# Kernel tuning notes

Measured on AMD Instinct MI355X. Metric: run time of the kernel, lower is better.

The kernel has to match this reference:

```python
import jax, jax.numpy as jnp
import numpy as np
from jax import lax

EPOCHS = 10  # self.epoch in the torch module


def setup_inputs() -> dict:
    key = jax.random.key(0)
    k1, k2 = jax.random.split(key)
    # (num_patches, groups, channels_per_group, kh, kw)
    patches = jax.random.normal(k1, (40000, 4, 16, 5, 5), dtype=jnp.float32)
    # torch: torch.randn([groups, K, D]) * 0.1
    centroids_init = jax.random.normal(k2, (4, 64, 400), dtype=jnp.float32) * 0.1
    return {"patches": patches, "centroids_init": centroids_init}


def reference(patches, centroids_init):
    N, G, C, H, W = patches.shape
    K = centroids_init.shape[1]
    D = C * H * W
    # [G, N, D] flattened patches per group
    pf = jnp.transpose(patches.reshape(N, G, D), (1, 0, 2))

    def step(centroids, _):
        # half squared norm of each centroid: [G, K]
        c2 = 0.5 * jnp.sum(centroids * centroids, axis=2)
        # scores[g,n,k] = <c_gk, p_gn> - 0.5||c_gk||^2  (max over k == nearest centroid)
        scores = jnp.einsum('gkd,gnd->gnk', centroids, pf) - c2[:, None, :]
        labels = jnp.argmax(scores, axis=2)                       # [G, N]
        S = jax.nn.one_hot(labels, K, dtype=pf.dtype)             # [G, N, K]
        summation = jnp.einsum('gnk,gnd->gkd', S, pf)             # [G, K, D]
        counts = jnp.sum(S, axis=1)                               # [G, K]
        new_c = summation / jnp.where(counts == 0, 1.0, counts)[:, :, None]
        # torch: centroids[:, where(counts==0)[1], :] = 0  -> zero that cluster
        # index across ALL groups if empty in any group
        bad = jnp.any(counts == 0, axis=0)                        # [K]
        new_c = jnp.where(bad[None, :, None], 0.0, new_c)
        return new_c, None

    centroids, _ = lax.scan(step, centroids_init, None, length=EPOCHS)
    # reshape to conv weight layout (out_channels, channels_per_group, kh, kw)
    return centroids.reshape(G * K, C, H, W)
```

## Files before the change

### kernel.cpp

```cpp
#include <hip/hip_runtime.h>

#define NPTS   40000
#define NG     4
#define NK     64
#define ND     400
#define PT     128
#define NCHUNK 25
#define NTILES 313
#define NSPL   16

typedef _Float16 f16x4 __attribute__((ext_vector_type(4)));
typedef float    f32x4 __attribute__((ext_vector_type(4)));

__global__ __launch_bounds__(256)
void assign_kernel(const float* __restrict__ patches,
                   const float* __restrict__ cent,
                   int*   __restrict__ lr,
                   int*   __restrict__ pcnt)
{
    const int g    = blockIdx.y;
    const int tile = blockIdx.x;
    const int t    = threadIdx.x;
    const int n0   = tile * PT;

    __shared__ _Float16 A1[PT][20];
    __shared__ _Float16 A2[PT][20];
    __shared__ _Float16 B1[NK][20];
    __shared__ _Float16 B2[NK][20];
    __shared__ float c2p[NK][4];
    __shared__ float c2s[NK];
    __shared__ int   cnt[NK];

    if (t < NK) cnt[t] = 0;

    {
        int k = t >> 2, j = t & 3;
        const float* c = cent + ((size_t)g * NK + k) * ND + 100 * j;
        float s = 0.0f;
        #pragma unroll
        for (int d = 0; d < 100; d += 4) {
            float4 v = *(const float4*)(c + d);
            s = fmaf(v.x, v.x, fmaf(v.y, v.y, fmaf(v.z, v.z, fmaf(v.w, v.w, s))));
        }
        c2p[k][j] = s;
    }
    __syncthreads();
    if (t < NK) c2s[t] = 2048.0f * (c2p[t][0] + c2p[t][1] + c2p[t][2] + c2p[t][3]);

    const int w   = t >> 6;
    const int l   = t & 63;
    const int q   = l >> 4;
    const int r15 = l & 15;

    const int rh = t & 127;
    const int hh = t >> 7;
    int nn = n0 + rh; if (nn >= NPTS) nn = NPTS - 1;
    const float* prow = patches + ((size_t)nn * NG + g) * ND + 8 * hh;
    const float* crow = cent + ((size_t)g * NK + (t >> 2)) * ND + 4 * (t & 3);

    f32x4 acc[2][4];
    {
        f32x4 z = {0.f, 0.f, 0.f, 0.f};
        #pragma unroll
        for (int i = 0; i < 2; ++i)
            #pragma unroll
            for (int j = 0; j < 4; ++j) acc[i][j] = z;
    }

    float4 pp[2]; float4 pc;
    pp[0] = *(const float4*)(prow);
    pp[1] = *(const float4*)(prow + 4);
    pc = *(const float4*)(crow);

    for (int c = 0; c < NCHUNK; ++c) {
        #pragma unroll
        for (int j2 = 0; j2 < 2; ++j2) {
            float4 v = pp[j2];
            float s0 = v.x * 64.0f, s1 = v.y * 64.0f, s2 = v.z * 64.0f, s3 = v.w * 64.0f;
            _Float16 a0 = (_Float16)s0, a1 = (_Float16)s1, a2 = (_Float16)s2, a3 = (_Float16)s3;
            f16x4 h1 = {a0, a1, a2, a3};
            f16x4 h2 = {(_Float16)(s0 - (float)a0), (_Float16)(s1 - (float)a1),
                        (_Float16)(s2 - (float)a2), (_Float16)(s3 - (float)a3)};
            *(f16x4*)&A1[rh][8 * hh + 4 * j2] = h1;
            *(f16x4*)&A2[rh][8 * hh + 4 * j2] = h2;
        }
        {
            float4 v = pc;
            float s0 = v.x * 64.0f, s1 = v.y * 64.0f, s2 = v.z * 64.0f, s3 = v.w * 64.0f;
            _Float16 a0 = (_Float16)s0, a1 = (_Float16)s1, a2 = (_Float16)s2, a3 = (_Float16)s3;
            f16x4 h1 = {a0, a1, a2, a3};
            f16x4 h2 = {(_Float16)(s0 - (float)a0), (_Float16)(s1 - (float)a1),
                        (_Float16)(s2 - (float)a2), (_Float16)(s3 - (float)a3)};
            int cc = t >> 2, jj = t & 3;
            *(f16x4*)&B1[cc][4 * jj] = h1;
            *(f16x4*)&B2[cc][4 * jj] = h2;
        }
        __syncthreads();

        if (c + 1 < NCHUNK) {
            const int d0 = (c + 1) * 16;
            pp[0] = *(const float4*)(prow + d0);
            pp[1] = *(const float4*)(prow + d0 + 4);
            pc = *(const float4*)(crow + d0);
        }

        f16x4 a1v[2], a2v[2], b1v[4], b2v[4];
        #pragma unroll
        for (int pi = 0; pi < 2; ++pi) {
            int p = 32 * w + 16 * pi + r15;
            a1v[pi] = *(const f16x4*)&A1[p][4 * q];
            a2v[pi] = *(const f16x4*)&A2[p][4 * q];
        }
        #pragma unroll
        for (int cj = 0; cj < 4; ++cj) {
            int n = 16 * cj + r15;
            b1v[cj] = *(const f16x4*)&B1[n][4 * q];
            b2v[cj] = *(const f16x4*)&B2[n][4 * q];
        }
        #pragma unroll
        for (int pi = 0; pi < 2; ++pi)
            #pragma unroll
            for (int cj = 0; cj < 4; ++cj) {
                acc[pi][cj] = __builtin_amdgcn_mfma_f32_16x16x16f16(a2v[pi], b1v[cj], acc[pi][cj], 0, 0, 0);
                acc[pi][cj] = __builtin_amdgcn_mfma_f32_16x16x16f16(a1v[pi], b2v[cj], acc[pi][cj], 0, 0, 0);
                acc[pi][cj] = __builtin_amdgcn_mfma_f32_16x16x16f16(a1v[pi], b1v[cj], acc[pi][cj], 0, 0, 0);
            }
        __syncthreads();
    }

    #pragma unroll
    for (int pi = 0; pi < 2; ++pi) {
        #pragma unroll
        for (int r = 0; r < 4; ++r) {
            float m  = acc[pi][0][r] - c2s[r15];
            int best = r15;
            #pragma unroll
            for (int cj = 1; cj < 4; ++cj) {
                int n = 16 * cj + r15;
                float s = acc[pi][cj][r] - c2s[n];
                if (s > m) { m = s; best = n; }
            }
            #pragma unroll
            for (int off = 1; off < 16; off <<= 1) {
                float om = __shfl_xor(m, off);
                int   ob = __shfl_xor(best, off);
                if (om > m || (om == m && ob < best)) { m = om; best = ob; }
            }
            if (r15 == 0) {
                int p  = 32 * w + 16 * pi + 4 * q + r;
                int np = n0 + p;
                if (np < NPTS) {
                    int rk = atomicAdd(&cnt[best], 1);
                    lr[(size_t)g * NPTS + np] = (rk << 8) | best;
                }
            }
        }
    }
    __syncthreads();
    if (t < NK) pcnt[((size_t)g * NTILES + tile) * NK + t] = cnt[t];
}

__global__ __launch_bounds__(256)
void scatter2_kernel(const int* __restrict__ lr,
                     const int* __restrict__ pcnt,
                     int* __restrict__ order,
                     int* __restrict__ cbase,
                     int* __restrict__ counts)
{
    const int tile = blockIdx.x, g = blockIdx.y, t = threadIdx.x;
    __shared__ unsigned short cnt_tk[NTILES * NK];
    __shared__ int part [4][NK];
    __shared__ int part2[4][NK];
    __shared__ int kbase[NK];
    __shared__ int tpre[NK];

    const int* pg = pcnt + (size_t)g * NTILES * NK;
    for (int i = t; i < NTILES * NK; i += 256)
        cnt_tk[i] = (unsigned short)pg[i];
    __syncthreads();

    {
        int k = t & 63, p = t >> 6;
        int s1 = 0, s2 = 0;
        for (int tl = p; tl < NTILES; tl += 4) {
            int v = cnt_tk[tl * NK + k];
            s1 += v;
            if (tl < tile) s2 += v;
        }
        part [p][k] = s1;
        part2[p][k] = s2;
    }
    __syncthreads();
    if (t < NK) {
        part[0][t] = part[0][t] + part[1][t] + part[2][t] + part[3][t];
        tpre[t]    = part2[0][t] + part2[1][t] + part2[2][t] + part2[3][t];
    }
    __syncthreads();
    if (t == 0) {
        int run = 0;
        for (int k = 0; k < NK; ++k) { kbase[k] = run; run += part[0][k]; }
    }
    __syncthreads();
    if (tile == 0 && t < NK) {
        cbase[g * NK + t]  = kbase[t];
        counts[g * NK + t] = part[0][t];
    }
    const int n = tile * PT + t;
    if (t < PT && n < NPTS) {
        int packed = lr[(size_t)g * NPTS + n];
        int L = packed & 63, r = packed >> 8;
        order[(size_t)g * NPTS + kbase[L] + tpre[L] + r] = n;
    }
}

__global__ __launch_bounds__(512, 2)
void gather_kernel(const float* __restrict__ patches,
                   const int*   __restrict__ order,
                   const int*   __restrict__ cbase,
                   const int*   __restrict__ counts,
                   float* __restrict__ psum)
{
    const int s = blockIdx.x, k = blockIdx.y, g = blockIdx.z;
    const int t = threadIdx.x;
    const int base = cbase[g * NK + k];
    const int cnt  = counts[g * NK + k];
    const int start = base + (cnt * s) / NSPL;
    const int end   = base + (cnt * (s + 1)) / NSPL;

    const int slot = t / 100;
    const int q    = t - slot * 100;

    float4 acc = make_float4(0.f, 0.f, 0.f, 0.f);
    if (t < 500) {
        const int* ord = order + (size_t)g * NPTS;
        #pragma unroll 4
        for (int i = start + slot; i < end; i += 5) {
            int n = ord[i];
            float4 v = *(const float4*)(patches + ((size_t)n * NG + g) * ND + 4 * q);
            acc.x += v.x; acc.y += v.y; acc.z += v.z; acc.w += v.w;
        }
    }

    __shared__ float sums[ND];
    for (int i = t; i < ND; i += 512) sums[i] = 0.0f;
    __syncthreads();
    if (t < 500) {
        atomicAdd(&sums[4 * q + 0], acc.x);
        atomicAdd(&sums[4 * q + 1], acc.y);
        atomicAdd(&sums[4 * q + 2], acc.z);
        atomicAdd(&sums[4 * q + 3], acc.w);
    }
    __syncthreads();
    if (t < 100) {
        float* dst = psum + (((size_t)(g * NK + k)) * NSPL + s) * ND + 4 * t;
        *(float4*)dst = *(const float4*)&sums[4 * t];
    }
}

__global__ __launch_bounds__(128)
void update_kernel(const float* __restrict__ psum,
                   const int*   __restrict__ counts,
                   float* __restrict__ outc)
{
    const int gk = blockIdx.x;
    const int g = gk >> 6, k = gk & 63;
    const int t = threadIdx.x;

    const bool bad = (counts[0 * NK + k] == 0) | (counts[1 * NK + k] == 0) |
                     (counts[2 * NK + k] == 0) | (counts[3 * NK + k] == 0);
    const int  c  = counts[g * NK + k];
    const float inv = 1.0f / (float)(c == 0 ? 1 : c);

    if (t < 100) {
        float4 s = make_float4(0.f, 0.f, 0.f, 0.f);
        const float* p = psum + ((size_t)gk * NSPL) * ND + 4 * t;
        #pragma unroll
        for (int sp = 0; sp < NSPL; ++sp) {
            float4 v = *(const float4*)(p + (size_t)sp * ND);
            s.x += v.x; s.y += v.y; s.z += v.z; s.w += v.w;
        }
        float4 o;
        o.x = bad ? 0.0f : s.x * inv;
        o.y = bad ? 0.0f : s.y * inv;
        o.z = bad ? 0.0f : s.z * inv;
        o.w = bad ? 0.0f : s.w * inv;
        *(float4*)(outc + (size_t)gk * ND + 4 * t) = o;
    }
}

extern "C" void kernel_launch(void* const* d_in, const int* in_sizes, int n_in,
                              void* d_out, int out_size, void* d_ws, size_t ws_size,
                              hipStream_t stream)
{
    const float* patches = (const float*)d_in[0];
    const float* cinit   = (const float*)d_in[1];
    float* out = (float*)d_out;

    const size_t CSZ = (size_t)NG * NK * ND;
    float* centA = (float*)d_ws;
    float* centB = centA + CSZ;
    int* lr       = (int*)(centB + CSZ);
    int* pcnt     = lr + (size_t)NG * NPTS;
    int* cbase    = pcnt + (size_t)NG * NTILES * NK;
    int* counts   = cbase + NG * NK;
    int* order    = counts + NG * NK;
    float* psum   = (float*)(order + (size_t)NG * NPTS);

    const float* cur = cinit;
    for (int e = 0; e < 10; ++e) {
        assign_kernel<<<dim3(NTILES, NG), 256, 0, stream>>>(patches, cur, lr, pcnt);
        scatter2_kernel<<<dim3(NTILES, NG), 256, 0, stream>>>(lr, pcnt, order, cbase, counts);
        gather_kernel<<<dim3(NSPL, NK, NG), 512, 0, stream>>>(patches, order, cbase, counts, psum);
        float* nxt = (e == 9) ? out : ((e & 1) ? centB : centA);
        update_kernel<<<dim3(NG * NK), 128, 0, stream>>>(psum, counts, nxt);
        cur = nxt;
    }
}
```

Measured before the change: 1.723 ms.

## Precompute fp16 hi/lo patch split and replace per-tile count scan with global atomics

Adds a one-time prepass that converts patches into scaled fp16 hi/lo pairs. The assign and gather kernels read these pairs directly, so the split is no longer recomputed in every epoch. Update writes the next centroids in the same split form. Cluster ranks now come from global atomic counters, which removes the per-tile count buffer and the heavy scan in which every scatter block reread all tile counts. The cost is an extra full pass over patches up front, contention on 256 global counters, and a point order within each cluster that is no longer deterministic.

Result: slower. 4.297 ms (+149.4%).

```diff
diff --git a/kernel.cpp b/kernel.cpp
--- a/kernel.cpp
+++ b/kernel.cpp
@@ -4,6 +4,7 @@
 #define NG     4
 #define NK     64
 #define ND     400
+#define NQ     100
 #define PT     128
 #define NCHUNK 25
 #define NTILES 313
@@ -12,11 +13,41 @@
 typedef _Float16 f16x4 __attribute__((ext_vector_type(4)));
 typedef float    f32x4 __attribute__((ext_vector_type(4)));
 
+struct __align__(16) HL { f16x4 hi; f16x4 lo; };
+
+__device__ __forceinline__ HL split4(float4 v) {
+    float s0 = v.x * 64.0f, s1 = v.y * 64.0f, s2 = v.z * 64.0f, s3 = v.w * 64.0f;
+    _Float16 a0 = (_Float16)s0, a1 = (_Float16)s1, a2 = (_Float16)s2, a3 = (_Float16)s3;
+    HL h;
+    h.hi = f16x4{a0, a1, a2, a3};
+    h.lo = f16x4{(_Float16)(s0 - (float)a0), (_Float16)(s1 - (float)a1),
+                 (_Float16)(s2 - (float)a2), (_Float16)(s3 - (float)a3)};
+    return h;
+}
+
 __global__ __launch_bounds__(256)
-void assign_kernel(const float* __restrict__ patches,
+void prepass_kernel(const float* __restrict__ patches, HL* __restrict__ ps)
+{
+    const int total = NPTS * NG * NQ;
+    for (int i = blockIdx.x * 256 + threadIdx.x; i < total; i += gridDim.x * 256)
+        ps[i] = split4(((const float4*)patches)[i]);
+}
+
+__global__ __launch_bounds__(128)
+void centprep_kernel(const float* __restrict__ cent, HL* __restrict__ cs,
+                     int* __restrict__ gcntbuf)
+{
+    const int gk = blockIdx.x, t = threadIdx.x;
+    if (t < NQ) cs[gk * NQ + t] = split4(((const float4*)cent)[gk * NQ + t]);
+    if (gk < 20 && t < 128) gcntbuf[gk * 128 + t] = 0;
+}
+
+__global__ __launch_bounds__(256)
+void assign_kernel(const HL* __restrict__ ps,
                    const float* __restrict__ cent,
+                   const HL* __restrict__ cs,
                    int*   __restrict__ lr,
-                   int*   __restrict__ pcnt)
+                   int*   __restrict__ gcnt)
 {
     const int g    = blockIdx.y;
     const int tile = blockIdx.x;
@@ -29,9 +60,6 @@
     __shared__ _Float16 B2[NK][20];
     __shared__ float c2p[NK][4];
     __shared__ float c2s[NK];
-    __shared__ int   cnt[NK];
-
-    if (t < NK) cnt[t] = 0;
 
     {
         int k = t >> 2, j = t & 3;
@@ -55,8 +83,9 @@
     const int rh = t & 127;
     const int hh = t >> 7;
     int nn = n0 + rh; if (nn >= NPTS) nn = NPTS - 1;
-    const float* prow = patches + ((size_t)nn * NG + g) * ND + 8 * hh;
-    const float* crow = cent + ((size_t)g * NK + (t >> 2)) * ND + 4 * (t & 3);
+    const HL* prow = ps + ((size_t)nn * NG + g) * NQ;
+    const HL* crow = cs + ((size_t)g * NK + (t >> 2)) * NQ;
+    const int jj = t & 3;
 
     f32x4 acc[2][4];
     {
@@ -67,41 +96,27 @@
             for (int j = 0; j < 4; ++j) acc[i][j] = z;
     }
 
-    float4 pp[2]; float4 pc;
-    pp[0] = *(const float4*)(prow);
-    pp[1] = *(const float4*)(prow + 4);
-    pc = *(const float4*)(crow);
+    HL ha0 = prow[2 * hh];
+    HL ha1 = prow[2 * hh + 1];
+    HL hb  = crow[jj];
 
     for (int c = 0; c < NCHUNK; ++c) {
-        #pragma unroll
-        for (int j2 = 0; j2 < 2; ++j2) {
-            float4 v = pp[j2];
-            float s0 = v.x * 64.0f, s1 = v.y * 64.0f, s2 = v.z * 64.0f, s3 = v.w * 64.0f;
-            _Float16 a0 = (_Float16)s0, a1 = (_Float16)s1, a2 = (_Float16)s2, a3 = (_Float16)s3;
-            f16x4 h1 = {a0, a1, a2, a3};
-            f16x4 h2 = {(_Float16)(s0 - (float)a0), (_Float16)(s1 - (float)a1),
-                        (_Float16)(s2 - (float)a2), (_Float16)(s3 - (float)a3)};
-            *(f16x4*)&A1[rh][8 * hh + 4 * j2] = h1;
-            *(f16x4*)&A2[rh][8 * hh + 4 * j2] = h2;
-        }
+        *(f16x4*)&A1[rh][8 * hh]     = ha0.hi;
+        *(f16x4*)&A2[rh][8 * hh]     = ha0.lo;
+        *(f16x4*)&A1[rh][8 * hh + 4] = ha1.hi;
+        *(f16x4*)&A2[rh][8 * hh + 4] = ha1.lo;
         {
-            float4 v = pc;
-            float s0 = v.x * 64.0f, s1 = v.y * 64.0f, s2 = v.z * 64.0f, s3 = v.w * 64.0f;
-            _Float16 a0 = (_Float16)s0, a1 = (_Float16)s1, a2 = (_Float16)s2, a3 = (_Float16)s3;
-            f16x4 h1 = {a0, a1, a2, a3};
-            f16x4 h2 = {(_Float16)(s0 - (float)a0), (_Float16)(s1 - (float)a1),
-                        (_Float16)(s2 - (float)a2), (_Float16)(s3 - (float)a3)};
-            int cc = t >> 2, jj = t & 3;
-            *(f16x4*)&B1[cc][4 * jj] = h1;
-            *(f16x4*)&B2[cc][4 * jj] = h2;
+            int cc = t >> 2;
+            *(f16x4*)&B1[cc][4 * jj] = hb.hi;
+            *(f16x4*)&B2[cc][4 * jj] = hb.lo;
         }
         __syncthreads();
 
         if (c + 1 < NCHUNK) {
-            const int d0 = (c + 1) * 16;
-            pp[0] = *(const float4*)(prow + d0);
-            pp[1] = *(const float4*)(prow + d0 + 4);
-            pc = *(const float4*)(crow + d0);
+            const int q0 = 4 * (c + 1);
+            ha0 = prow[q0 + 2 * hh];
+            ha1 = prow[q0 + 2 * hh + 1];
+            hb  = crow[q0 + jj];
         }
 
         f16x4 a1v[2], a2v[2], b1v[4], b2v[4];
@@ -150,80 +165,51 @@
                 int p  = 32 * w + 16 * pi + 4 * q + r;
                 int np = n0 + p;
                 if (np < NPTS) {
-                    int rk = atomicAdd(&cnt[best], 1);
-                    lr[(size_t)g * NPTS + np] = (rk << 8) | best;
+                    int rk = atomicAdd(&gcnt[g * NK + best], 1);
+                    lr[(size_t)g * NPTS + np] = (rk << 6) | best;
                 }
             }
         }
     }
-    __syncthreads();
-    if (t < NK) pcnt[((size_t)g * NTILES + tile) * NK + t] = cnt[t];
-}
-
-__global__ __launch_bounds__(256)
-void scatter2_kernel(const int* __restrict__ lr,
-                     const int* __restrict__ pcnt,
-                     int* __restrict__ order,
-                     int* __restrict__ cbase,
-                     int* __restrict__ counts)
+}
+
+__global__ __launch_bounds__(128)
+void scatter_kernel(const int* __restrict__ lr,
+                    const int* __restrict__ gcnt,
+                    int* __restrict__ order)
 {
     const int tile = blockIdx.x, g = blockIdx.y, t = threadIdx.x;
-    __shared__ unsigned short cnt_tk[NTILES * NK];
-    __shared__ int part [4][NK];
-    __shared__ int part2[4][NK];
-    __shared__ int kbase[NK];
-    __shared__ int tpre[NK];
-
-    const int* pg = pcnt + (size_t)g * NTILES * NK;
-    for (int i = t; i < NTILES * NK; i += 256)
-        cnt_tk[i] = (unsigned short)pg[i];
-    __syncthreads();
-
-    {
-        int k = t & 63, p = t >> 6;
-        int s1 = 0, s2 = 0;
-        for (int tl = p; tl < NTILES; tl += 4) {
-            int v = cnt_tk[tl * NK + k];
-            s1 += v;
-            if (tl < tile) s2 += v;
-        }
-        part [p][k] = s1;
-        part2[p][k] = s2;
-    }
-    __syncthreads();
-    if (t < NK) {
-        part[0][t] = part[0][t] + part[1][t] + part[2][t] + part[3][t];
-        tpre[t]    = part2[0][t] + part2[1][t] + part2[2][t] + part2[3][t];
-    }
-    __syncthreads();
+    __shared__ int kb[NK];
     if (t == 0) {
         int run = 0;
-        for (int k = 0; k < NK; ++k) { kbase[k] = run; run += part[0][k]; }
-    }
-    __syncthreads();
-    if (tile == 0 && t < NK) {
-        cbase[g * NK + t]  = kbase[t];
-        counts[g * NK + t] = part[0][t];
-    }
+        for (int k = 0; k < NK; ++k) { kb[k] = run; run += gcnt[g * NK + k]; }
+    }
+    __syncthreads();
     const int n = tile * PT + t;
-    if (t < PT && n < NPTS) {
+    if (n < NPTS) {
         int packed = lr[(size_t)g * NPTS + n];
-        int L = packed & 63, r = packed >> 8;
-        order[(size_t)g * NPTS + kbase[L] + tpre[L] + r] = n;
+        int L = packed & 63, r = packed >> 6;
+        order[(size_t)g * NPTS + kb[L] + r] = n;
     }
 }
 
 __global__ __launch_bounds__(512, 2)
-void gather_kernel(const float* __restrict__ patches,
-                   const int*   __restrict__ order,
-                   const int*   __restrict__ cbase,
-                   const int*   __restrict__ counts,
+void gather_kernel(const HL*  __restrict__ ps,
+                   const int* __restrict__ order,
+                   const int* __restrict__ gcnt,
                    float* __restrict__ psum)
 {
     const int s = blockIdx.x, k = blockIdx.y, g = blockIdx.z;
     const int t = threadIdx.x;
-    const int base = cbase[g * NK + k];
-    const int cnt  = counts[g * NK + k];
+
+    __shared__ int sb[2];
+    if (t == 0) {
+        int b = 0;
+        for (int i = 0; i < k; ++i) b += gcnt[g * NK + i];
+        sb[0] = b; sb[1] = gcnt[g * NK + k];
+    }
+    __syncthreads();
+    const int base = sb[0], cnt = sb[1];
     const int start = base + (cnt * s) / NSPL;
     const int end   = base + (cnt * (s + 1)) / NSPL;
 
@@ -233,11 +219,14 @@
     float4 acc = make_float4(0.f, 0.f, 0.f, 0.f);
     if (t < 500) {
         const int* ord = order + (size_t)g * NPTS;
-        #pragma unroll 4
+        #pragma unroll 2
         for (int i = start + slot; i < end; i += 5) {
             int n = ord[i];
-            float4 v = *(const float4*)(patches + ((size_t)n * NG + g) * ND + 4 * q);
-            acc.x += v.x; acc.y += v.y; acc.z += v.z; acc.w += v.w;
+            HL h = ps[((size_t)n * NG + g) * NQ + q];
+            acc.x += (float)h.hi[0] + (float)h.lo[0];
+            acc.y += (float)h.hi[1] + (float)h.lo[1];
+            acc.z += (float)h.hi[2] + (float)h.lo[2];
+            acc.w += (float)h.hi[3] + (float)h.lo[3];
         }
     }
 
@@ -259,19 +248,20 @@
 
 __global__ __launch_bounds__(128)
 void update_kernel(const float* __restrict__ psum,
-                   const int*   __restrict__ counts,
-                   float* __restrict__ outc)
+                   const int*   __restrict__ gcnt,
+                   float* __restrict__ outc,
+                   HL*    __restrict__ cs)
 {
     const int gk = blockIdx.x;
     const int g = gk >> 6, k = gk & 63;
     const int t = threadIdx.x;
 
-    const bool bad = (counts[0 * NK + k] == 0) | (counts[1 * NK + k] == 0) |
-                     (counts[2 * NK + k] == 0) | (counts[3 * NK + k] == 0);
-    const int  c  = counts[g * NK + k];
+    const bool bad = (gcnt[0 * NK + k] == 0) | (gcnt[1 * NK + k] == 0) |
+                     (gcnt[2 * NK + k] == 0) | (gcnt[3 * NK + k] == 0);
+    const int  c  = gcnt[g * NK + k];
     const float inv = 1.0f / (float)(c == 0 ? 1 : c);
 
-    if (t < 100) {
+    if (t < NQ) {
         float4 s = make_float4(0.f, 0.f, 0.f, 0.f);
         const float* p = psum + ((size_t)gk * NSPL) * ND + 4 * t;
         #pragma unroll
@@ -279,12 +269,21 @@
             float4 v = *(const float4*)(p + (size_t)sp * ND);
             s.x += v.x; s.y += v.y; s.z += v.z; s.w += v.w;
         }
-        float4 o;
-        o.x = bad ? 0.0f : s.x * inv;
-        o.y = bad ? 0.0f : s.y * inv;
-        o.z = bad ? 0.0f : s.z * inv;
-        o.w = bad ? 0.0f : s.w * inv;
+        float4 c64;
+        c64.x = bad ? 0.0f : s.x * inv;
+        c64.y = bad ? 0.0f : s.y * inv;
+        c64.z = bad ? 0.0f : s.z * inv;
+        c64.w = bad ? 0.0f : s.w * inv;
+        float4 o = make_float4(c64.x * 0.015625f, c64.y * 0.015625f,
+                               c64.z * 0.015625f, c64.w * 0.015625f);
         *(float4*)(outc + (size_t)gk * ND + 4 * t) = o;
+        _Float16 a0 = (_Float16)c64.x, a1 = (_Float16)c64.y,
+                 a2 = (_Float16)c64.z, a3 = (_Float16)c64.w;
+        HL h;
+        h.hi = f16x4{a0, a1, a2, a3};
+        h.lo = f16x4{(_Float16)(c64.x - (float)a0), (_Float16)(c64.y - (float)a1),
+                     (_Float16)(c64.z - (float)a2), (_Float16)(c64.w - (float)a3)};
+        cs[(size_t)gk * NQ + t] = h;
     }
 }
 
@@ -296,23 +295,27 @@
     const float* cinit   = (const float*)d_in[1];
     float* out = (float*)d_out;
 
-    const size_t CSZ = (size_t)NG * NK * ND;
-    float* centA = (float*)d_ws;
-    float* centB = centA + CSZ;
-    int* lr       = (int*)(centB + CSZ);
-    int* pcnt     = lr + (size_t)NG * NPTS;
-    int* cbase    = pcnt + (size_t)NG * NTILES * NK;
-    int* counts   = cbase + NG * NK;
-    int* order    = counts + NG * NK;
-    float* psum   = (float*)(order + (size_t)NG * NPTS);
+    char* wp = (char*)d_ws;
+    HL* PS = (HL*)wp;               wp += (size_t)NPTS * NG * NQ * sizeof(HL);
+    HL* CS = (HL*)wp;               wp += (size_t)NG * NK * NQ * sizeof(HL);
+    float* centA = (float*)wp;      wp += (size_t)NG * NK * ND * 4;
+    float* centB = (float*)wp;      wp += (size_t)NG * NK * ND * 4;
+    int* lr      = (int*)wp;        wp += (size_t)NG * NPTS * 4;
+    int* order   = (int*)wp;        wp += (size_t)NG * NPTS * 4;
+    int* gcntbuf = (int*)wp;        wp += 2560 * 4;
+    float* psum  = (float*)wp;
+
+    prepass_kernel<<<4096, 256, 0, stream>>>(patches, PS);
+    centprep_kernel<<<NG * NK, 128, 0, stream>>>(cinit, CS, gcntbuf);
 
     const float* cur = cinit;
     for (int e = 0; e < 10; ++e) {
-        assign_kernel<<<dim3(NTILES, NG), 256, 0, stream>>>(patches, cur, lr, pcnt);
-        scatter2_kernel<<<dim3(NTILES, NG), 256, 0, stream>>>(lr, pcnt, order, cbase, counts);
-        gather_kernel<<<dim3(NSPL, NK, NG), 512, 0, stream>>>(patches, order, cbase, counts, psum);
+        int* gc = gcntbuf + 256 * e;
+        assign_kernel<<<dim3(NTILES, NG), 256, 0, stream>>>(PS, cur, CS, lr, gc);
+        scatter_kernel<<<dim3(NTILES, NG), 128, 0, stream>>>(lr, gc, order);
+        gather_kernel<<<dim3(NSPL, NK, NG), 512, 0, stream>>>(PS, order, gc, psum);
         float* nxt = (e == 9) ? out : ((e & 1) ? centB : centA);
-        update_kernel<<<dim3(NG * NK), 128, 0, stream>>>(psum, counts, nxt);
+        update_kernel<<<NG * NK, 128, 0, stream>>>(psum, gc, nxt, CS);
         cur = nxt;
     }
 }
```
